# Kernel tuning notes

Measured on AMD Instinct MI355X. Metric: run time of the kernel, lower is better.

## Reference

```python
import jax, jax.numpy as jnp
import numpy as np

N_EMBD = 1024
D_FF = 4096
N_EXPERTS = 8
TOP_K = 2


def setup_inputs() -> dict:
    key = jax.random.key(0)
    k1, k2, k3, k4 = jax.random.split(key, 4)
    x = jax.random.normal(k1, (1, 2048, N_EMBD), dtype=jnp.float32)
    mask = jnp.ones((2048, N_EXPERTS), dtype=jnp.float32)
    Wr = jax.random.normal(k2, (N_EMBD, N_EXPERTS), dtype=jnp.float32) * 0.02
    W1 = jax.random.normal(k3, (N_EXPERTS, N_EMBD, D_FF), dtype=jnp.float32) * 0.02
    W2 = jax.random.normal(k4, (N_EXPERTS, D_FF, N_EMBD), dtype=jnp.float32) * 0.02
    return {"x": x, "mask": mask, "Wr": Wr, "W1": W1, "W2": W2}


def reference(x, mask, Wr, W1, W2):
    T = x.shape[0] * x.shape[1]
    xs = x.reshape(T, N_EMBD)                      # [T, d]
    router_logits = (xs @ Wr) * mask               # [T, E], masked as in MaskedMoE
    all_probs = jax.nn.softmax(router_logits, axis=-1)  # softmax_topk order
    weights, selected = jax.lax.top_k(all_probs, TOP_K)  # [T, K]
    # combine[t, e] = sum of routing weights where token t selected expert e
    combine = jnp.zeros((T, N_EXPERTS), dtype=xs.dtype)
    combine = combine.at[jnp.arange(T)[:, None], selected].add(weights)
    results = jnp.zeros_like(xs)
    for e in range(N_EXPERTS):  # fixed small expert count
        h = jax.nn.gelu(xs @ W1[e])                # [T, d_ff]
        out = h @ W2[e]                            # [T, d]
        results = results + combine[:, e:e + 1] * out
    return results.reshape(x.shape)
```

## Files before the change

### kernel.cpp

```cpp
#include <hip/hip_runtime.h>
#include <hip/hip_bf16.h>


#define T_TOK 2048
#define D_EMB 1024
#define DFF   4096
#define NE    8

typedef _Float16 f16x8 __attribute__((ext_vector_type(8)));
typedef float    f32x4 __attribute__((ext_vector_type(4)));

__device__ __forceinline__ float gelu_tanh(float x) {
    const float c = 0.7978845608028654f;
    float z = c * (x + 0.044715f * x * x * x);
    float u = __expf(2.0f * z);
    return 0.5f * x * (1.0f + (u - 1.0f) / (u + 1.0f));
}

__device__ __forceinline__ void gll(const void* g, void* l) {
    __builtin_amdgcn_global_load_lds((__attribute__((address_space(1))) void*)g,
                                     (__attribute__((address_space(3))) void*)l,
                                     16, 0, 0);
}

__global__ void k_zero(int* counts) {
    if (threadIdx.x < NE) counts[threadIdx.x] = 0;
}

__global__ __launch_bounds__(256) void k_router(
    const float* __restrict__ x, const float* __restrict__ mask,
    const float* __restrict__ Wr, _Float16* __restrict__ xh,
    int* __restrict__ counts, int* __restrict__ elist,
    int* __restrict__ tok_e, int* __restrict__ tok_p, float* __restrict__ tok_w) {
    int wave = threadIdx.x >> 6;
    int lane = threadIdx.x & 63;
    int t = blockIdx.x * 4 + wave;
    if (t >= T_TOK) return;

    float acc[NE];
#pragma unroll
    for (int e = 0; e < NE; e++) acc[e] = 0.f;
    const float* xr = x + (size_t)t * D_EMB;
    for (int c = 0; c < D_EMB / 64; c++) {
        int i = c * 64 + lane;
        float xv = xr[i];
        xh[(size_t)t * D_EMB + i] = (_Float16)xv;
        const float* wr = Wr + (size_t)i * NE;
#pragma unroll
        for (int e = 0; e < NE; e++) acc[e] += xv * wr[e];
    }
#pragma unroll
    for (int e = 0; e < NE; e++) {
#pragma unroll
        for (int off = 32; off > 0; off >>= 1)
            acc[e] += __shfl_xor(acc[e], off);
    }
    if (lane == 0) {
        float p[NE];
        float mx = -1e30f;
#pragma unroll
        for (int e = 0; e < NE; e++) {
            p[e] = acc[e] * mask[t * NE + e];
            mx = fmaxf(mx, p[e]);
        }
        float s = 0.f;
#pragma unroll
        for (int e = 0; e < NE; e++) { p[e] = expf(p[e] - mx); s += p[e]; }
#pragma unroll
        for (int e = 0; e < NE; e++) p[e] /= s;
        int e0 = 0; float b0 = p[0];
#pragma unroll
        for (int e = 1; e < NE; e++) if (p[e] > b0) { b0 = p[e]; e0 = e; }
        int e1 = -1; float b1 = -1.f;
#pragma unroll
        for (int e = 0; e < NE; e++) if (e != e0 && p[e] > b1) { b1 = p[e]; e1 = e; }

        int pos0 = atomicAdd(&counts[e0], 1);
        elist[e0 * T_TOK + pos0] = t;
        tok_e[t * 2 + 0] = e0; tok_p[t * 2 + 0] = pos0; tok_w[t * 2 + 0] = b0;
        int pos1 = atomicAdd(&counts[e1], 1);
        elist[e1 * T_TOK + pos1] = t;
        tok_e[t * 2 + 1] = e1; tok_p[t * 2 + 1] = pos1; tok_w[t * 2 + 1] = b1;
    }
}

__global__ __launch_bounds__(256) void k_transpose(
    const float* __restrict__ W1, const float* __restrict__ W2,
    _Float16* __restrict__ W1T, _Float16* __restrict__ W2T) {
    __shared__ float tile[64 * 132];
    int bz = blockIdx.z;
    int e = bz & 7;
    bool isW2 = bz >= 8;
    const float* S = (isW2 ? W2 : W1) + (size_t)e * 4194304;
    _Float16* Dst = (isW2 ? W2T : W1T) + (size_t)e * 4194304;
    int src_ld   = isW2 ? 1024 : 4096;
    int plane_sz = isW2 ? 65536 : 262144;
    int bx = blockIdx.x;
    int kt, nb;
    if (isW2) { kt = bx >> 3; nb = (bx & 7) * 128; }
    else      { kt = bx >> 5; nb = (bx & 31) * 128; }
    int kb = kt * 64;
    int tid = threadIdx.x;

#pragma unroll
    for (int i = 0; i < 8; i++) {
        int f = i * 256 + tid;
        int row = f >> 5;
        int col4 = f & 31;
        float4 v = *(const float4*)(S + (size_t)(kb + row) * src_ld + nb + col4 * 4);
        int col4s = col4 ^ ((row >> 3) & 7);
        *(float4*)(&tile[row * 132 + col4s * 4]) = v;
    }
    __syncthreads();

    _Float16* plane = Dst + (size_t)kt * plane_sz;
#pragma unroll
    for (int i = 0; i < 4; i++) {
        int idx = i * 256 + tid;
        int n = idx >> 3;
        int c = idx & 7;
        f16x8 o;
#pragma unroll
        for (int u = 0; u < 8; u++) {
            int k = c * 8 + u;
            int col4s = (n >> 2) ^ ((k >> 3) & 7);
            o[u] = (_Float16)tile[k * 132 + col4s * 4 + (n & 3)];
        }
        *(f16x8*)(plane + (size_t)(nb + n) * 64 + (c ^ (n & 7)) * 8) = o;
    }
}


__global__ __launch_bounds__(256) void k_gemm1(
    const _Float16* __restrict__ xh, const _Float16* __restrict__ BT,
    const int* __restrict__ counts, const int* __restrict__ elist,
    _Float16* __restrict__ H) {
    int e = blockIdx.z;
    int cnt = counts[e];
    int p0 = blockIdx.y * 128;
    if (p0 >= cnt) return;
    int rowbase = 0;
    for (int i = 0; i < NE; i++) rowbase += (i < e) ? counts[i] : 0;
    int n0 = blockIdx.x * 128;
    const _Float16* B = BT + (size_t)e * 4194304;

    __shared__ _Float16 As[128 * 64];
    __shared__ _Float16 Bs[128 * 64];
    __shared__ int ttok[128];

    int tid = threadIdx.x;
    if (tid < 128) ttok[tid] = elist[e * T_TOK + min(p0 + tid, cnt - 1)];
    __syncthreads();

    int w = tid >> 6, lane = tid & 63;
    int rq = tid >> 3;
    int cch = (tid & 7) ^ ((tid >> 3) & 7);
    const _Float16* pA[4];
    const _Float16* pB[4];
    _Float16* lA[4];
    _Float16* lB[4];
#pragma unroll
    for (int q = 0; q < 4; q++) {
        int row = q * 32 + rq;
        pA[q] = xh + (size_t)ttok[row] * D_EMB + cch * 8;
        pB[q] = B + (size_t)n0 * 64 + (q * 256 + tid) * 8;
        lA[q] = As + (q * 256 + w * 64) * 8;
        lB[q] = Bs + (q * 256 + w * 64) * 8;
    }

    int wm = w >> 1, wn = w & 1;
    int lhi = lane >> 4, llo = lane & 15;
    int m7 = llo & 7;
    int kc0 = lhi ^ m7, kc1 = kc0 ^ 4;
    const _Float16* arp0 = As + (wm * 64 + llo) * 64 + kc0 * 8;
    const _Float16* arp1 = As + (wm * 64 + llo) * 64 + kc1 * 8;
    const _Float16* brp0 = Bs + (wn * 64 + llo) * 64 + kc0 * 8;
    const _Float16* brp1 = Bs + (wn * 64 + llo) * 64 + kc1 * 8;

    f32x4 acc[4][4] = {};
    for (int it = 0; it < 16; ++it) {
        __syncthreads();
#pragma unroll
        for (int q = 0; q < 4; q++) { gll(pA[q], lA[q]); gll(pB[q], lB[q]); }
#pragma unroll
        for (int q = 0; q < 4; q++) { pA[q] += 64; pB[q] += 262144; }
        __syncthreads();
        f16x8 a[4], b[4];
#pragma unroll
        for (int i = 0; i < 4; i++) {
            a[i] = *(const f16x8*)(arp0 + i * 1024);
            b[i] = *(const f16x8*)(brp0 + i * 1024);
        }
#pragma unroll
        for (int mt = 0; mt < 4; mt++)
#pragma unroll
            for (int nt = 0; nt < 4; nt++)
                acc[mt][nt] = __builtin_amdgcn_mfma_f32_16x16x32_f16(a[mt], b[nt], acc[mt][nt], 0, 0, 0);
#pragma unroll
        for (int i = 0; i < 4; i++) {
            a[i] = *(const f16x8*)(arp1 + i * 1024);
            b[i] = *(const f16x8*)(brp1 + i * 1024);
        }
#pragma unroll
        for (int mt = 0; mt < 4; mt++)
#pragma unroll
            for (int nt = 0; nt < 4; nt++)
                acc[mt][nt] = __builtin_amdgcn_mfma_f32_16x16x32_f16(a[mt], b[nt], acc[mt][nt], 0, 0, 0);
    }

#pragma unroll
    for (int mt = 0; mt < 4; mt++) {
#pragma unroll
        for (int i = 0; i < 4; i++) {
            int p = p0 + wm * 64 + mt * 16 + lhi * 4 + i;
            if (p < cnt) {
                size_t rowoff = (size_t)(rowbase + p) * DFF + n0 + wn * 64 + llo;
#pragma unroll
                for (int nt = 0; nt < 4; nt++)
                    H[rowoff + nt * 16] = (_Float16)gelu_tanh(acc[mt][nt][i]);
            }
        }
    }
}

__global__ __launch_bounds__(256) void k_gemm2(
    const _Float16* __restrict__ H, const _Float16* __restrict__ BT,
    const int* __restrict__ counts, float* __restrict__ Obase) {
    int bz = blockIdx.z;
    int e = bz & 7, sp = bz >> 3;
    int cnt = counts[e];
    int p0 = blockIdx.y * 128;
    if (p0 >= cnt) return;
    int rowbase = 0;
    for (int i = 0; i < NE; i++) rowbase += (i < e) ? counts[i] : 0;
    int n0 = blockIdx.x * 128;
    int kh = sp * 1024;
    const _Float16* B = BT + (size_t)e * 4194304;
    float* O = Obase + (size_t)sp * 4194304;

    __shared__ _Float16 As[128 * 64];
    __shared__ _Float16 Bs[128 * 64];

    int tid = threadIdx.x;
    int w = tid >> 6, lane = tid & 63;
    int rq = tid >> 3;
    int cch = (tid & 7) ^ ((tid >> 3) & 7);
    const _Float16* pA[4];
    const _Float16* pB[4];
    _Float16* lA[4];
    _Float16* lB[4];
#pragma unroll
    for (int q = 0; q < 4; q++) {
        int row = q * 32 + rq;
        int r = rowbase + min(p0 + row, cnt - 1);
        pA[q] = H + (size_t)r * DFF + kh + cch * 8;
        pB[q] = B + (size_t)(sp * 16) * 65536 + (size_t)n0 * 64 + (q * 256 + tid) * 8;
        lA[q] = As + (q * 256 + w * 64) * 8;
        lB[q] = Bs + (q * 256 + w * 64) * 8;
    }

    int wm = w >> 1, wn = w & 1;
    int lhi = lane >> 4, llo = lane & 15;
    int m7 = llo & 7;
    int kc0 = lhi ^ m7, kc1 = kc0 ^ 4;
    const _Float16* arp0 = As + (wm * 64 + llo) * 64 + kc0 * 8;
    const _Float16* arp1 = As + (wm * 64 + llo) * 64 + kc1 * 8;
    const _Float16* brp0 = Bs + (wn * 64 + llo) * 64 + kc0 * 8;
    const _Float16* brp1 = Bs + (wn * 64 + llo) * 64 + kc1 * 8;

    f32x4 acc[4][4] = {};
    for (int it = 0; it < 16; ++it) {
        __syncthreads();
#pragma unroll
        for (int q = 0; q < 4; q++) { gll(pA[q], lA[q]); gll(pB[q], lB[q]); }
#pragma unroll
        for (int q = 0; q < 4; q++) { pA[q] += 64; pB[q] += 65536; }
        __syncthreads();
        f16x8 a[4], b[4];
#pragma unroll
        for (int i = 0; i < 4; i++) {
            a[i] = *(const f16x8*)(arp0 + i * 1024);
            b[i] = *(const f16x8*)(brp0 + i * 1024);
        }
#pragma unroll
        for (int mt = 0; mt < 4; mt++)
#pragma unroll
            for (int nt = 0; nt < 4; nt++)
                acc[mt][nt] = __builtin_amdgcn_mfma_f32_16x16x32_f16(a[mt], b[nt], acc[mt][nt], 0, 0, 0);
#pragma unroll
        for (int i = 0; i < 4; i++) {
            a[i] = *(const f16x8*)(arp1 + i * 1024);
            b[i] = *(const f16x8*)(brp1 + i * 1024);
        }
#pragma unroll
        for (int mt = 0; mt < 4; mt++)
#pragma unroll
            for (int nt = 0; nt < 4; nt++)
                acc[mt][nt] = __builtin_amdgcn_mfma_f32_16x16x32_f16(a[mt], b[nt], acc[mt][nt], 0, 0, 0);
    }

#pragma unroll
    for (int mt = 0; mt < 4; mt++) {
#pragma unroll
        for (int i = 0; i < 4; i++) {
            int p = p0 + wm * 64 + mt * 16 + lhi * 4 + i;
            if (p < cnt) {
                size_t o = (size_t)(rowbase + p) * D_EMB + n0 + wn * 64 + llo;
#pragma unroll
                for (int nt = 0; nt < 4; nt++)
                    O[o + nt * 16] = acc[mt][nt][i];
            }
        }
    }
}

__global__ __launch_bounds__(256) void k_final(
    const float* __restrict__ Obase, const int* __restrict__ counts,
    const int* __restrict__ tok_e, const int* __restrict__ tok_p,
    const float* __restrict__ tok_w, float* __restrict__ out) {
    __shared__ int sb[NE];
    int t = blockIdx.x;
    if (threadIdx.x == 0) {
        int s = 0;
        for (int e = 0; e < NE; e++) { sb[e] = s; s += counts[e]; }
    }
    __syncthreads();
    int r0 = sb[tok_e[t * 2 + 0]] + tok_p[t * 2 + 0];
    int r1 = sb[tok_e[t * 2 + 1]] + tok_p[t * 2 + 1];
    float w0 = tok_w[t * 2 + 0], w1 = tok_w[t * 2 + 1];
    int i = threadIdx.x * 4;
    float4 s0 = {0, 0, 0, 0}, s1 = {0, 0, 0, 0};
#pragma unroll
    for (int sp = 0; sp < 4; sp++) {
        const float* O = Obase + (size_t)sp * 4194304;
        float4 a = *(const float4*)(O + (size_t)r0 * D_EMB + i);
        float4 b = *(const float4*)(O + (size_t)r1 * D_EMB + i);
        s0.x += a.x; s0.y += a.y; s0.z += a.z; s0.w += a.w;
        s1.x += b.x; s1.y += b.y; s1.z += b.z; s1.w += b.w;
    }
    float4 o;
    o.x = w0 * s0.x + w1 * s1.x;
    o.y = w0 * s0.y + w1 * s1.y;
    o.z = w0 * s0.z + w1 * s1.z;
    o.w = w0 * s0.w + w1 * s1.w;
    *(float4*)(out + (size_t)t * D_EMB + i) = o;
}

extern "C" void kernel_launch(void* const* d_in, const int* in_sizes, int n_in,
                              void* d_out, int out_size, void* d_ws, size_t ws_size,
                              hipStream_t stream) {
    const float* x    = (const float*)d_in[0];
    const float* mask = (const float*)d_in[1];
    const float* Wr   = (const float*)d_in[2];
    const float* W1   = (const float*)d_in[3];
    const float* W2   = (const float*)d_in[4];
    float* out = (float*)d_out;

    char* ws = (char*)d_ws;
    const size_t MB = 1024 * 1024;
    int*      counts = (int*)(ws + 0);
    int*      elist  = (int*)(ws + 1024);
    int*      tok_e  = (int*)(ws + 1024 + 65536);
    int*      tok_p  = (int*)(ws + 1024 + 65536 + 16384);
    float*    tok_w  = (float*)(ws + 1024 + 65536 + 32768);
    _Float16* xh     = (_Float16*)(ws + 1 * MB);
    _Float16* W1T    = (_Float16*)(ws + 8 * MB);
    _Float16* W2T    = (_Float16*)(ws + 72 * MB);
    _Float16* H      = (_Float16*)(ws + 136 * MB);
    float*    Obuf   = (float*)(ws + 168 * MB);

    k_zero<<<1, 64, 0, stream>>>(counts);
    k_router<<<T_TOK / 4, 256, 0, stream>>>(x, mask, Wr, xh, counts, elist, tok_e, tok_p, tok_w);
    k_transpose<<<dim3(512, 1, 16), 256, 0, stream>>>(W1, W2, W1T, W2T);
    k_gemm1<<<dim3(32, 16, NE), 256, 0, stream>>>(xh, W1T, counts, elist, H);
    k_gemm2<<<dim3(8, 16, 32), 256, 0, stream>>>(H, W2T, counts, Obuf);
    k_final<<<T_TOK, 256, 0, stream>>>(Obuf, counts, tok_e, tok_p, tok_w, out);
}
```

Before: 496.7 us.

## Transpose weights in registers into k-chunk-major fp16 layout for conflict-free B reads

```diff
diff --git a/kernel.cpp b/kernel.cpp
--- a/kernel.cpp
+++ b/kernel.cpp
@@ -87,47 +87,39 @@
 __global__ __launch_bounds__(256) void k_transpose(
     const float* __restrict__ W1, const float* __restrict__ W2,
     _Float16* __restrict__ W1T, _Float16* __restrict__ W2T) {
-    __shared__ float tile[64 * 132];
     int bz = blockIdx.z;
     int e = bz & 7;
     bool isW2 = bz >= 8;
     const float* S = (isW2 ? W2 : W1) + (size_t)e * 4194304;
     _Float16* Dst = (isW2 ? W2T : W1T) + (size_t)e * 4194304;
-    int src_ld   = isW2 ? 1024 : 4096;
-    int plane_sz = isW2 ? 65536 : 262144;
+    int ld      = isW2 ? 1024 : 4096;
+    int ktplane = isW2 ? 65536 : 262144;
     int bx = blockIdx.x;
-    int kt, nb;
-    if (isW2) { kt = bx >> 3; nb = (bx & 7) * 128; }
-    else      { kt = bx >> 5; nb = (bx & 31) * 128; }
-    int kb = kt * 64;
-    int tid = threadIdx.x;
-
-#pragma unroll
-    for (int i = 0; i < 8; i++) {
-        int f = i * 256 + tid;
-        int row = f >> 5;
-        int col4 = f & 31;
-        float4 v = *(const float4*)(S + (size_t)(kb + row) * src_ld + nb + col4 * 4);
-        int col4s = col4 ^ ((row >> 3) & 7);
-        *(float4*)(&tile[row * 132 + col4s * 4]) = v;
-    }
-    __syncthreads();
-
-    _Float16* plane = Dst + (size_t)kt * plane_sz;
-#pragma unroll
-    for (int i = 0; i < 4; i++) {
-        int idx = i * 256 + tid;
-        int n = idx >> 3;
-        int c = idx & 7;
-        f16x8 o;
-#pragma unroll
-        for (int u = 0; u < 8; u++) {
-            int k = c * 8 + u;
-            int col4s = (n >> 2) ^ ((k >> 3) & 7);
-            o[u] = (_Float16)tile[k * 132 + col4s * 4 + (n & 3)];
-        }
-        *(f16x8*)(plane + (size_t)(nb + n) * 64 + (c ^ (n & 7)) * 8) = o;
-    }
+    int g, nb;
+    if (isW2) { g = bx; nb = 0; }
+    else      { g = bx >> 2; nb = (bx & 3) * 1024; }
+
+    int t = threadIdx.x;
+    int n = nb + t * 4;
+    const float* src = S + (size_t)(g * 8) * ld + n;
+
+    f32x4 v[8];
+#pragma unroll
+    for (int r = 0; r < 8; r++)
+        v[r] = *(const f32x4*)(src + (size_t)r * ld);
+
+    f16x8 o[4];
+#pragma unroll
+    for (int j = 0; j < 4; j++)
+#pragma unroll
+        for (int u = 0; u < 8; u++)
+            o[j][u] = (_Float16)v[u][j];
+
+    size_t off = (size_t)(g >> 3) * ktplane + (size_t)(n >> 7) * 8192
+               + (g & 7) * 1024 + (n & 127) * 8;
+    f16x8* d = (f16x8*)(Dst + off);
+#pragma unroll
+    for (int j = 0; j < 4; j++) d[j] = o[j];
 }
 
 
@@ -174,8 +166,8 @@
     int kc0 = lhi ^ m7, kc1 = kc0 ^ 4;
     const _Float16* arp0 = As + (wm * 64 + llo) * 64 + kc0 * 8;
     const _Float16* arp1 = As + (wm * 64 + llo) * 64 + kc1 * 8;
-    const _Float16* brp0 = Bs + (wn * 64 + llo) * 64 + kc0 * 8;
-    const _Float16* brp1 = Bs + (wn * 64 + llo) * 64 + kc1 * 8;
+    const _Float16* brp0 = Bs + (lhi * 128 + wn * 64 + llo) * 8;
+    const _Float16* brp1 = Bs + ((lhi + 4) * 128 + wn * 64 + llo) * 8;
 
     f32x4 acc[4][4] = {};
     for (int it = 0; it < 16; ++it) {
@@ -189,7 +181,7 @@
 #pragma unroll
         for (int i = 0; i < 4; i++) {
             a[i] = *(const f16x8*)(arp0 + i * 1024);
-            b[i] = *(const f16x8*)(brp0 + i * 1024);
+            b[i] = *(const f16x8*)(brp0 + i * 128);
         }
 #pragma unroll
         for (int mt = 0; mt < 4; mt++)
@@ -199,7 +191,7 @@
 #pragma unroll
         for (int i = 0; i < 4; i++) {
             a[i] = *(const f16x8*)(arp1 + i * 1024);
-            b[i] = *(const f16x8*)(brp1 + i * 1024);
+            b[i] = *(const f16x8*)(brp1 + i * 128);
         }
 #pragma unroll
         for (int mt = 0; mt < 4; mt++)
@@ -265,8 +257,8 @@
     int kc0 = lhi ^ m7, kc1 = kc0 ^ 4;
     const _Float16* arp0 = As + (wm * 64 + llo) * 64 + kc0 * 8;
     const _Float16* arp1 = As + (wm * 64 + llo) * 64 + kc1 * 8;
-    const _Float16* brp0 = Bs + (wn * 64 + llo) * 64 + kc0 * 8;
-    const _Float16* brp1 = Bs + (wn * 64 + llo) * 64 + kc1 * 8;
+    const _Float16* brp0 = Bs + (lhi * 128 + wn * 64 + llo) * 8;
+    const _Float16* brp1 = Bs + ((lhi + 4) * 128 + wn * 64 + llo) * 8;
 
     f32x4 acc[4][4] = {};
     for (int it = 0; it < 16; ++it) {
@@ -280,7 +272,7 @@
 #pragma unroll
         for (int i = 0; i < 4; i++) {
             a[i] = *(const f16x8*)(arp0 + i * 1024);
-            b[i] = *(const f16x8*)(brp0 + i * 1024);
+            b[i] = *(const f16x8*)(brp0 + i * 128);
         }
 #pragma unroll
         for (int mt = 0; mt < 4; mt++)
@@ -290,7 +282,7 @@
 #pragma unroll
         for (int i = 0; i < 4; i++) {
             a[i] = *(const f16x8*)(arp1 + i * 1024);
-            b[i] = *(const f16x8*)(brp1 + i * 1024);
+            b[i] = *(const f16x8*)(brp1 + i * 128);
         }
 #pragma unroll
         for (int mt = 0; mt < 4; mt++)
```

New measurement: 504.7 us. No clear change (+1.6%).
